# Performance work log

Measured on AMD Instinct MI355X. Metric: run time of the kernel, lower is better.

Reference implementation:

```python
import jax, jax.numpy as jnp
import numpy as np
import math

LOG2PI = math.log(2.0 * math.pi)


def _pair_sum(m1, v1, m2, v2, w):
    """sum_{i,j} w[i,j] * exp(delta_ij) for diagonal 2-D Gaussians.

    m1,v1: [K1,2] means / diagonal variances; m2,v2: [K2,2]; w: [K1,K2].
    Closed form of the torch code's 2x2 inverse/det/mm chain exploiting the
    fact that all covariances are diagonal (cov = diag((wh/2)^2)).
    """
    ci = 1.0 / v1[:, None, :]                      # [K1,1,2] = cov_inv_i diag
    cj = 1.0 / v2[None, :, :]                      # [1,K2,2] = cov_inv_j diag
    s = ci + cj                                    # [K1,K2,2] = cov_inv_ij diag
    mij = (m1[:, None, :] * ci + m2[None, :, :] * cj) / s   # combined mean
    quad = (jnp.sum(mij * mij * s, -1)
            - jnp.sum(m1 * m1 / v1, -1)[:, None]
            - jnp.sum(m2 * m2 / v2, -1)[None, :])            # [K1,K2]
    # log(det(cov_inv_ij) / (det(cov_inv_i) * det(cov_inv_j)))
    logdet = (jnp.sum(jnp.log(s), -1)
              + jnp.sum(jnp.log(v1), -1)[:, None]
              + jnp.sum(jnp.log(v2), -1)[None, :])           # [K1,K2]
    delta = 0.5 * (quad - logdet - 2.0 * LOG2PI)   # x_dim = 2
    return jnp.sum(w * jnp.exp(delta))


def _cs_div(p_m, p_v, p_a, q_m, q_v, q_a):
    pq = _pair_sum(p_m, p_v, q_m, q_v, p_a @ q_a.T)
    pp = _pair_sum(p_m, p_v, p_m, p_v, p_a @ p_a.T)
    qq = _pair_sum(q_m, q_v, q_m, q_v, q_a @ q_a.T)
    return 2.0 * jnp.log(pq) - jnp.log(pp) - jnp.log(qq)


def _forward(pred_bboxes, pred_labels, gt_bboxes, gt_labels):
    num_classes = pred_labels.shape[2] - 1
    pred_alpha = (jax.nn.sigmoid(pred_labels[:, :, -1])[:, :, None]
                  * jax.nn.softmax(pred_labels[:, :, :-1], axis=2))   # [bs,kp,C]
    gt_alpha = jax.nn.one_hot(gt_labels, num_classes, dtype=pred_alpha.dtype)
    pred_m = pred_bboxes[:, :, :2]
    pred_v = jnp.square(pred_bboxes[:, :, 2:] / 2.0)
    gt_m = gt_bboxes[:, :, :2]
    gt_v = jnp.square(gt_bboxes[:, :, 2:] / 2.0)
    per_img = jax.vmap(_cs_div)(gt_m, gt_v, gt_alpha, pred_m, pred_v, pred_alpha)
    return -jnp.sum(per_img)


def setup_inputs() -> dict:
    key = jax.random.key(0)
    k1, k2, k3, k4 = jax.random.split(key, 4)
    BS, KP, KG, NC = 32, 1000, 100, 80
    # widths/heights must be strictly positive -> uniform in [0.05, 1)
    pred_bboxes = jax.random.uniform(k1, (BS, KP, 4), jnp.float32, 0.05, 1.0)
    pred_labels = jax.random.normal(k2, (BS, KP, NC + 1), jnp.float32)
    gt_bboxes = jax.random.uniform(k3, (BS, KG, 4), jnp.float32, 0.05, 1.0)
    gt_labels = jax.random.randint(k4, (BS, KG), 0, NC)
    return {"pred_bboxes": pred_bboxes, "pred_labels": pred_labels,
            "gt_bboxes": gt_bboxes, "gt_labels": gt_labels}


def reference(pred_bboxes, pred_labels, gt_bboxes, gt_labels):
    return _forward(pred_bboxes, pred_labels, gt_bboxes, gt_labels)
```

## Files before the change

kernel.cpp:

```cpp
#include <hip/hip_runtime.h>
#include <math.h>

#define BS 32
#define KP 1000
#define KPP 1024
#define KG 100
#define NC 80
#define SK 96
#define LP 104
#define NT 8
#define NPAIR 36
#define NQQ (BS * NPAIR)
#define NPPQ (5 * BS)
#define NALL (NQQ + NPPQ)

using bf16x8 = __attribute__((ext_vector_type(8))) short;
using f32x4  = __attribute__((ext_vector_type(4))) float;
using f32x2  = __attribute__((ext_vector_type(2))) float;

__device__ __forceinline__ float wave_reduce_sum(float v) {
#pragma unroll
    for (int m = 32; m > 0; m >>= 1) v += __shfl_xor(v, m, 64);
    return v;
}
__device__ __forceinline__ float wave_reduce_max(float v) {
#pragma unroll
    for (int m = 32; m > 0; m >>= 1) v = fmaxf(v, __shfl_xor(v, m, 64));
    return v;
}

__device__ __forceinline__ unsigned short f2bf(float f) {
    unsigned int u = __float_as_uint(f);
    u += 0x7fffu + ((u >> 16) & 1u);
    return (unsigned short)(u >> 16);
}
__device__ __forceinline__ float bf2f(unsigned short h) {
    return __uint_as_float(((unsigned int)h) << 16);
}

__device__ __forceinline__ float kval(float4 a, float4 b) {
    f32x2 S = (f32x2){a.z, a.w} + (f32x2){b.z, b.w};
    f32x2 d = (f32x2){a.x, a.y} - (f32x2){b.x, b.y};
    f32x2 d2 = d * d;
    f32x2 t = d2 * S.yx;
    float num = t.x + t.y;
    float P = S.x * S.y;
    float rs = __builtin_amdgcn_rsqf(P);
    float q = num * rs * rs;
    return 0.15915494309189535f * rs * __expf(-0.5f * q);
}

__global__ __launch_bounds__(256) void alpha_kernel(const float* __restrict__ pl,
                                                    unsigned short* __restrict__ ah,
                                                    float* __restrict__ acc) {
    if (blockIdx.x == 0 && threadIdx.x < 128) acc[threadIdx.x] = 0.0f;
    int wave = threadIdx.x >> 6;
    int lane = threadIdx.x & 63;
    int rr = blockIdx.x * 4 + wave;
    int b = rr >> 10, r = rr & (KPP - 1);
    unsigned short* oh = ah + (size_t)rr * SK;
    if (r < KP) {
        const float* x = pl + ((size_t)b * KP + r) * (NC + 1);
        float l0 = x[lane];
        float l1 = (lane < 16) ? x[64 + lane] : -1e30f;
        float obj = x[NC];
        float m = wave_reduce_max(fmaxf(l0, l1));
        float e0 = __expf(l0 - m);
        float e1 = (lane < 16) ? __expf(l1 - m) : 0.0f;
        float s = wave_reduce_sum(e0 + e1);
        float sig = 1.0f / (1.0f + __expf(-obj));
        float sc = sig / s;
        oh[lane] = f2bf(e0 * sc);
        if (lane < 32) oh[64 + lane] = (lane < 16) ? f2bf(e1 * sc) : 0;
    } else {
        oh[lane] = 0;
        if (lane < 32) oh[64 + lane] = 0;
    }
}

__global__ __launch_bounds__(256, 3) void main_kernel(const float* __restrict__ pb,
                                                      const unsigned short* __restrict__ ahg,
                                                      const float* __restrict__ gtb,
                                                      const int* __restrict__ gtl,
                                                      float* __restrict__ acc,
                                                      float* __restrict__ out) {
    __shared__ short la[128 * LP];
    __shared__ short lbb[128 * LP];
    __shared__ float red[4];
    __shared__ int last;

    int tid = threadIdx.x;
    int lane = tid & 63, w = tid >> 6;
    int bi = blockIdx.x;

    if (bi < NPPQ) {
        int b = bi & 31;
        int p5 = bi >> 5;
        float4* gm = (float4*)lbb;
        int* gl = (int*)la;
        if (tid < KG) {
            float4 x = ((const float4*)gtb)[b * KG + tid];
            gm[tid] = make_float4(x.x, x.y, 0.25f * x.z * x.z, 0.25f * x.w * x.w);
            gl[tid] = gtl[b * KG + tid];
        }
        __syncthreads();
        float part = 0.0f;
        if (p5 < 4) {
            int j = p5 * 256 + tid;
            if (j < KP) {
                float4 x = ((const float4*)pb)[b * KP + j];
                float4 pm = make_float4(x.x, x.y, 0.25f * x.z * x.z, 0.25f * x.w * x.w);
                const unsigned short* rh = ahg + ((size_t)(b << 10) + j) * SK;
#pragma unroll 4
                for (int i = 0; i < KG; ++i) {
                    part += bf2f(rh[gl[i]]) * kval(gm[i], pm);
                }
            }
        } else {
            for (int p = tid; p < KG * KG; p += 256) {
                int i = p / KG;
                int j = p - i * KG;
                if (gl[i] == gl[j]) part += kval(gm[i], gm[j]);
            }
        }
        part = wave_reduce_sum(part);
        if (lane == 0) red[w] = part;
        __syncthreads();
        if (tid == 0) {
            float s = red[0] + red[1] + red[2] + red[3];
            atomicAdd((p5 < 4) ? &acc[b] : &acc[32 + b], s);
        }
    } else {
        int qi = bi - NPPQ;
        int b = qi & 31;
        int t = qi >> 5;
        int it = 0, rem = t;
        while (rem >= NT - it) { rem -= NT - it; ++it; }
        int jt = it + rem;
        int i0 = it * 128, j0 = jt * 128;

        {
            int side = tid >> 7, r = tid & 127;
            int gi = (side ? j0 : i0) + r;
            float4 v = make_float4(0.0f, 0.0f, 1.0f, 1.0f);
            if (gi < KP) {
                float4 x = ((const float4*)pb)[b * KP + gi];
                v = make_float4(x.x, x.y, 0.25f * x.z * x.z, 0.25f * x.w * x.w);
            }
            short* L = side ? lbb : la;
            *(float4*)(L + r * LP + 96) = v;
        }

        {
            const float4* sa = (const float4*)(ahg + ((size_t)(b << 10) + i0) * SK);
#pragma unroll
            for (int k = 0; k < 6; ++k) {
                int o = tid + k * 256;
                int row = o / 12, slot = o - row * 12;
                *(float4*)(la + row * LP + slot * 8) = sa[o];
            }
            if (jt != it) {
                const float4* sb = (const float4*)(ahg + ((size_t)(b << 10) + j0) * SK);
#pragma unroll
                for (int k = 0; k < 6; ++k) {
                    int o = tid + k * 256;
                    int row = o / 12, slot = o - row * 12;
                    *(float4*)(lbb + row * LP + slot * 8) = sb[o];
                }
            }
        }
        __syncthreads();
        const short* LB = (jt != it) ? lbb : la;

        int wy = w >> 1, wx = w & 1;
        int m15 = lane & 15, quad = lane >> 4;
        int ar = wy * 64 + m15;
        int br = wx * 64 + m15;

        f32x4 c4[4][4];
#pragma unroll
        for (int r = 0; r < 4; ++r)
#pragma unroll
            for (int s = 0; s < 4; ++s) c4[r][s] = (f32x4){0.0f, 0.0f, 0.0f, 0.0f};

#pragma unroll
        for (int ks = 0; ks < 3; ++ks) {
            int kk = ks * 32 + quad * 8;
            bf16x8 bh[4];
#pragma unroll
            for (int cg = 0; cg < 4; ++cg)
                bh[cg] = *(const bf16x8*)(LB + (br + cg * 16) * LP + kk);
#pragma unroll
            for (int rg = 0; rg < 4; ++rg) {
                bf16x8 xh = *(const bf16x8*)(la + (ar + rg * 16) * LP + kk);
#pragma unroll
                for (int cg = 0; cg < 4; ++cg)
                    c4[rg][cg] = __builtin_amdgcn_mfma_f32_16x16x32_bf16(xh, bh[cg], c4[rg][cg], 0, 0, 0);
            }
        }

        float4 pj[4];
        int jb = wx * 64 + m15;
#pragma unroll
        for (int cg = 0; cg < 4; ++cg)
            pj[cg] = *(const float4*)(lbb + (jb + cg * 16) * LP + 96);
        float part = 0.0f;
        int ib = wy * 64 + quad * 4;
#pragma unroll
        for (int rg = 0; rg < 4; ++rg) {
#pragma unroll
            for (int e = 0; e < 4; ++e) {
                float4 pi = *(const float4*)(la + (ib + rg * 16 + e) * LP + 96);
#pragma unroll
                for (int cg = 0; cg < 4; ++cg)
                    part += c4[rg][cg][e] * kval(pi, pj[cg]);
            }
        }
        if (jt != it) part *= 2.0f;

        part = wave_reduce_sum(part);
        if (lane == 0) red[w] = part;
        __syncthreads();
        if (tid == 0)
            atomicAdd(&acc[64 + b], red[0] + red[1] + red[2] + red[3]);
    }

    if (tid == 0) {
        __threadfence();
        unsigned int o = atomicAdd((unsigned int*)(acc + 96), 1u);
        last = (o == NALL - 1) ? 1 : 0;
    }
    __syncthreads();
    if (last && tid < 64) {
        float v = 0.0f;
        if (tid < BS) {
            float pq = atomicAdd(&acc[tid], 0.0f);
            float pp = atomicAdd(&acc[32 + tid], 0.0f);
            float qq = atomicAdd(&acc[64 + tid], 0.0f);
            v = 2.0f * logf(pq) - logf(pp) - logf(qq);
        }
        v = wave_reduce_sum(v);
        if (tid == 0) out[0] = -v;
    }
}

extern "C" void kernel_launch(void* const* d_in, const int* in_sizes, int n_in,
                              void* d_out, int out_size, void* d_ws, size_t ws_size,
                              hipStream_t stream) {
    (void)in_sizes; (void)n_in; (void)out_size; (void)ws_size;
    const float* pred_bb  = (const float*)d_in[0];
    const float* pred_lab = (const float*)d_in[1];
    const float* gt_bb    = (const float*)d_in[2];
    const int*   gt_lab   = (const int*)d_in[3];
    float* out = (float*)d_out;

    unsigned short* ah = (unsigned short*)d_ws;
    float* acc = (float*)(ah + (size_t)BS * KPP * SK);

    hipLaunchKernelGGL(alpha_kernel, dim3(BS * KPP / 4), dim3(256), 0, stream,
                       pred_lab, ah, acc);
    hipLaunchKernelGGL(main_kernel, dim3(NALL), dim3(256), 0, stream,
                       pred_bb, ah, gt_bb, gt_lab, acc, out);
}
```

Measured before the change: 106.3 us.

## Stage alpha rows in LDS, reorder block roles, and spread atomic accumulators

The pred-gt blocks now copy their 256 alpha rows from global memory into LDS with coalesced float4 loads. Before, each thread gathered scattered bf16 values straight from global memory. The qq tile blocks now get the low block indices and the pq/pp blocks run last. Per-image accumulators are padded to a 16-float stride, and completion uses a two-level counter (per image, then global) to cut contention on a single atomic. The cost is extra LDS traffic and an extra sync for the gather blocks.

```diff
diff --git a/kernel.cpp b/kernel.cpp
--- a/kernel.cpp
+++ b/kernel.cpp
@@ -13,6 +13,8 @@
 #define NQQ (BS * NPAIR)
 #define NPPQ (5 * BS)
 #define NALL (NQQ + NPPQ)
+#define NPERIMG 41
+#define GCNT 512
 
 using bf16x8 = __attribute__((ext_vector_type(8))) short;
 using f32x4  = __attribute__((ext_vector_type(4))) float;
@@ -53,7 +55,10 @@
 __global__ __launch_bounds__(256) void alpha_kernel(const float* __restrict__ pl,
                                                     unsigned short* __restrict__ ah,
                                                     float* __restrict__ acc) {
-    if (blockIdx.x == 0 && threadIdx.x < 128) acc[threadIdx.x] = 0.0f;
+    if (blockIdx.x == 0) {
+#pragma unroll
+        for (int k = 0; k < 3; ++k) acc[threadIdx.x + 256 * k] = 0.0f;
+    }
     int wave = threadIdx.x >> 6;
     int lane = threadIdx.x & 63;
     int rr = blockIdx.x * 4 + wave;
@@ -84,55 +89,20 @@
                                                       const int* __restrict__ gtl,
                                                       float* __restrict__ acc,
                                                       float* __restrict__ out) {
-    __shared__ short la[128 * LP];
-    __shared__ short lbb[128 * LP];
+    __shared__ short lds[2 * 128 * LP];
     __shared__ float red[4];
     __shared__ int last;
 
     int tid = threadIdx.x;
     int lane = tid & 63, w = tid >> 6;
     int bi = blockIdx.x;
-
-    if (bi < NPPQ) {
-        int b = bi & 31;
-        int p5 = bi >> 5;
-        float4* gm = (float4*)lbb;
-        int* gl = (int*)la;
-        if (tid < KG) {
-            float4 x = ((const float4*)gtb)[b * KG + tid];
-            gm[tid] = make_float4(x.x, x.y, 0.25f * x.z * x.z, 0.25f * x.w * x.w);
-            gl[tid] = gtl[b * KG + tid];
-        }
-        __syncthreads();
-        float part = 0.0f;
-        if (p5 < 4) {
-            int j = p5 * 256 + tid;
-            if (j < KP) {
-                float4 x = ((const float4*)pb)[b * KP + j];
-                float4 pm = make_float4(x.x, x.y, 0.25f * x.z * x.z, 0.25f * x.w * x.w);
-                const unsigned short* rh = ahg + ((size_t)(b << 10) + j) * SK;
-#pragma unroll 4
-                for (int i = 0; i < KG; ++i) {
-                    part += bf2f(rh[gl[i]]) * kval(gm[i], pm);
-                }
-            }
-        } else {
-            for (int p = tid; p < KG * KG; p += 256) {
-                int i = p / KG;
-                int j = p - i * KG;
-                if (gl[i] == gl[j]) part += kval(gm[i], gm[j]);
-            }
-        }
-        part = wave_reduce_sum(part);
-        if (lane == 0) red[w] = part;
-        __syncthreads();
-        if (tid == 0) {
-            float s = red[0] + red[1] + red[2] + red[3];
-            atomicAdd((p5 < 4) ? &acc[b] : &acc[32 + b], s);
-        }
-    } else {
-        int qi = bi - NPPQ;
-        int b = qi & 31;
+    int b;
+
+    if (bi < NQQ) {
+        short* la = lds;
+        short* lbb = lds + 128 * LP;
+        int qi = bi;
+        b = qi & 31;
         int t = qi >> 5;
         int it = 0, rem = t;
         while (rem >= NT - it) { rem -= NT - it; ++it; }
@@ -222,21 +192,74 @@
         if (lane == 0) red[w] = part;
         __syncthreads();
         if (tid == 0)
-            atomicAdd(&acc[64 + b], red[0] + red[1] + red[2] + red[3]);
+            atomicAdd(&acc[b * 16 + 2], red[0] + red[1] + red[2] + red[3]);
+    } else {
+        int pi = bi - NQQ;
+        b = pi & 31;
+        int p5 = pi >> 5;
+        short* lalpha = lds;
+        float4* gm = (float4*)(lds + 24576);
+        int* gl = (int*)(lds + 24576 + 800);
+        if (tid < KG) {
+            float4 x = ((const float4*)gtb)[b * KG + tid];
+            gm[tid] = make_float4(x.x, x.y, 0.25f * x.z * x.z, 0.25f * x.w * x.w);
+            gl[tid] = gtl[b * KG + tid];
+        }
+        if (p5 < 4) {
+            const float4* sa = (const float4*)(ahg + ((size_t)(b << 10) + p5 * 256) * SK);
+#pragma unroll
+            for (int k = 0; k < 12; ++k) {
+                int o = tid + k * 256;
+                *(float4*)(lalpha + o * 8) = sa[o];
+            }
+        }
+        __syncthreads();
+        float part = 0.0f;
+        if (p5 < 4) {
+            int j = p5 * 256 + tid;
+            if (j < KP) {
+                float4 x = ((const float4*)pb)[b * KP + j];
+                float4 pm = make_float4(x.x, x.y, 0.25f * x.z * x.z, 0.25f * x.w * x.w);
+                const unsigned short* arow = (const unsigned short*)lalpha + tid * SK;
+#pragma unroll 4
+                for (int i = 0; i < KG; ++i) {
+                    part += bf2f(arow[gl[i]]) * kval(gm[i], pm);
+                }
+            }
+        } else {
+            for (int p = tid; p < KG * KG; p += 256) {
+                int i = p / KG;
+                int j = p - i * KG;
+                if (gl[i] == gl[j]) part += kval(gm[i], gm[j]);
+            }
+        }
+        part = wave_reduce_sum(part);
+        if (lane == 0) red[w] = part;
+        __syncthreads();
+        if (tid == 0) {
+            float s = red[0] + red[1] + red[2] + red[3];
+            atomicAdd(&acc[b * 16 + ((p5 < 4) ? 0 : 1)], s);
+        }
     }
 
     if (tid == 0) {
         __threadfence();
-        unsigned int o = atomicAdd((unsigned int*)(acc + 96), 1u);
-        last = (o == NALL - 1) ? 1 : 0;
+        unsigned int o = atomicAdd((unsigned int*)(acc + b * 16 + 4), 1u);
+        int l = 0;
+        if (o == NPERIMG - 1) {
+            __threadfence();
+            unsigned int g = atomicAdd((unsigned int*)(acc + GCNT), 1u);
+            l = (g == BS - 1) ? 1 : 0;
+        }
+        last = l;
     }
     __syncthreads();
     if (last && tid < 64) {
         float v = 0.0f;
         if (tid < BS) {
-            float pq = atomicAdd(&acc[tid], 0.0f);
-            float pp = atomicAdd(&acc[32 + tid], 0.0f);
-            float qq = atomicAdd(&acc[64 + tid], 0.0f);
+            float pq = atomicAdd(&acc[tid * 16 + 0], 0.0f);
+            float pp = atomicAdd(&acc[tid * 16 + 1], 0.0f);
+            float qq = atomicAdd(&acc[tid * 16 + 2], 0.0f);
             v = 2.0f * logf(pq) - logf(pp) - logf(qq);
         }
         v = wave_reduce_sum(v);
```

Measured after the change: 105.3 us. Within noise of the previous version (-0.9%).
